# Kernel tuning notes

Hardware: AMD Instinct MI355X
Metric: run time of the kernel (lower is better)

The kernel has to match this reference:

```python
import jax, jax.numpy as jnp
import numpy as np
from jax import lax

WIN = 9
EPS = 1e-05


def _box_sum(v, win):
    # v: [B, 1, D, H, W]
    pad = win // 2
    dn = lax.conv_dimension_numbers(v.shape, (1, 1, win, win, win), ('NCDHW', 'OIDHW', 'NCDHW'))
    k = jnp.ones((win,), v.dtype)
    # apply 1D sum along D, H, W in turn
    v = lax.conv_general_dilated(v, k.reshape(1, 1, win, 1, 1), (1, 1, 1), [(pad, pad), (0, 0), (0, 0)], dimension_numbers=dn)
    v = lax.conv_general_dilated(v, k.reshape(1, 1, 1, win, 1), (1, 1, 1), [(0, 0), (pad, pad), (0, 0)], dimension_numbers=dn)
    v = lax.conv_general_dilated(v, k.reshape(1, 1, 1, 1, win), (1, 1, 1), [(0, 0), (0, 0), (pad, pad)], dimension_numbers=dn)
    return v


def setup_inputs() -> dict:
    key = jax.random.key(0)
    k1, k2 = jax.random.split(key)
    shape = (2, 1, 160, 192, 160)
    x = jax.random.uniform(k1, shape, dtype=jnp.float32)
    y = jax.random.uniform(k2, shape, dtype=jnp.float32)
    return {"x": x, "y": y}


def reference(x, y):
    win = WIN
    win_size = float(win ** 3)
    x_sum = _box_sum(x, win)
    y_sum = _box_sum(y, win)
    x2_sum = _box_sum(x * x, win)
    y2_sum = _box_sum(y * y, win)
    xy_sum = _box_sum(x * y, win)
    cross = xy_sum - x_sum * y_sum / win_size
    x_var = jnp.maximum(x2_sum - x_sum * x_sum / win_size, EPS)
    y_var = jnp.maximum(y2_sum - y_sum * y_sum / win_size, EPS)
    cc = cross * cross / (x_var * y_var)
    return -jnp.mean(cc)
```

## Files before the change

### kernel.cpp

```cpp
#include <hip/hip_runtime.h>

#define BB 2
#define DD 160
#define HH 192
#define WW 160
#define HW (HH * WW)
#define PAD 4
#define TH 16
#define TW 16
#define EXT 24
#define XSTR 28
#define PLANE 768
#define WCS 456
#define WJS 28
#define WPS (5 * WCS)
#define HWS 20
#define HCS2 324
#define CHUNK 55
#define NCH 3
#define NITER 63
#define WT (WW / TW)
#define HT (HH / TH)
#define NBLK (WT * HT * NCH * BB)
#define NTASK 288
#define EPS 1e-5f
#define INV_WS (1.0f / 729.0f)

__device__ __forceinline__ void bar_lgkm() {
  asm volatile("s_waitcnt lgkmcnt(0)" ::: "memory");
  __builtin_amdgcn_s_barrier();
  asm volatile("" ::: "memory");
}

__global__ void __launch_bounds__(256) k_lncc(
    const float* __restrict__ x, const float* __restrict__ y,
    float* __restrict__ partials)
{
  __shared__ __align__(16) float sbuf[2][PLANE];
  __shared__ __align__(16) float wsum[2 * WPS];
  __shared__ __align__(16) float hsum[5 * HCS2];
  __shared__ float red[4];

  const int t = threadIdx.x;
  const int w0 = blockIdx.x * TW;
  const int h0 = blockIdx.y * TH;
  const int bz = blockIdx.z;
  const int b = bz / NCH;
  const int chunk = bz - b * NCH;
  const int dc0 = chunk * CHUNK;
  const int g0 = dc0 - PAD;

  for (int i = t; i < 2 * PLANE; i += 256) (&sbuf[0][0])[i] = 0.f;

  int la0, la1; bool tk0, tk1;
  const float* gp0; const float* gp1;
  {
    const float* bx = x + (long)b * DD * HW;
    const float* by = y + (long)b * DD * HW;
#define MKTASK(TAU, LA, TK, GP)                                           \
    {                                                                     \
      int tau = (TAU);                                                    \
      int a = tau / 144;                                                  \
      int rem = tau - 144 * a;                                            \
      int r = rem / 6;                                                    \
      int q = rem - 6 * r;                                                \
      int aa = (a < 2) ? a : 0;                                           \
      int gh = h0 - PAD + r;                                              \
      int gw = w0 - PAD + 4 * q;                                          \
      bool ok = (tau < NTASK) && ((unsigned)gh < (unsigned)HH) &&         \
                ((unsigned)gw < (unsigned)WW);                            \
      LA = aa * PLANE + r * XSTR + 4 * q;                                 \
      TK = ok;                                                            \
      GP = (aa ? by : bx) + (ok ? (gh * WW + gw) : 0);                    \
    }
    MKTASK(t, la0, tk0, gp0)
    MKTASK(256 + t, la1, tk1, gp1)
#undef MKTASK
  }

  const int c2 = t / 24, r2 = t - c2 * 24;
  const int arrA = ((c2 == 1) || (c2 == 3)) ? 1 : 0;
  const bool needB = (c2 == 4);
  const bool sqA = (c2 == 2) || (c2 == 3);
  const int paOff = arrA * PLANE + r2 * XSTR;
  const int pbOff = PLANE + r2 * XSTR;
  const int wwOff = c2 * WCS + r2;

  const int tt = t - 128;
  const int c3 = (tt >= 0 ? tt : 0) / 16, w3 = (tt >= 0 ? tt : 0) & 15;
  const int wrOff = c3 * WCS + w3 * WJS;
  float* const hwr = &hsum[c3 * HCS2 + w3 * HWS];

  const int h4 = t >> 4, w4 = t & 15;
  const float* const hrd = &hsum[w4 * HWS + h4];

  float ring[9][5];
#pragma unroll
  for (int i = 0; i < 9; ++i)
#pragma unroll
    for (int c = 0; c < 5; ++c) ring[i][c] = 0.f;
  float run0 = 0.f, run1 = 0.f, run2 = 0.f, run3 = 0.f, run4 = 0.f, acc = 0.f;

  __syncthreads();

#define P2_BODY(PARBASE)                                                   \
  {                                                                        \
    const float* pa = &sbuf[0][0] + paOff;                                 \
    float4 A0 = *(const float4*)(pa);                                      \
    float4 A1 = *(const float4*)(pa + 4);                                  \
    float4 A2 = *(const float4*)(pa + 8);                                  \
    float4 A3 = *(const float4*)(pa + 12);                                 \
    float4 A4 = *(const float4*)(pa + 16);                                 \
    float4 A5 = *(const float4*)(pa + 20);                                 \
    float av[EXT];                                                         \
    av[0]=A0.x; av[1]=A0.y; av[2]=A0.z; av[3]=A0.w;                        \
    av[4]=A1.x; av[5]=A1.y; av[6]=A1.z; av[7]=A1.w;                        \
    av[8]=A2.x; av[9]=A2.y; av[10]=A2.z; av[11]=A2.w;                      \
    av[12]=A3.x; av[13]=A3.y; av[14]=A3.z; av[15]=A3.w;                    \
    av[16]=A4.x; av[17]=A4.y; av[18]=A4.z; av[19]=A4.w;                    \
    av[20]=A5.x; av[21]=A5.y; av[22]=A5.z; av[23]=A5.w;                    \
    float q[EXT];                                                          \
    if (needB) {                                                           \
      const float* pb = &sbuf[0][0] + pbOff;                               \
      float4 B0 = *(const float4*)(pb);                                    \
      float4 B1 = *(const float4*)(pb + 4);                                \
      float4 B2 = *(const float4*)(pb + 8);                                \
      float4 B3 = *(const float4*)(pb + 12);                               \
      float4 B4 = *(const float4*)(pb + 16);                               \
      float4 B5 = *(const float4*)(pb + 20);                               \
      q[0]=av[0]*B0.x; q[1]=av[1]*B0.y; q[2]=av[2]*B0.z; q[3]=av[3]*B0.w;  \
      q[4]=av[4]*B1.x; q[5]=av[5]*B1.y; q[6]=av[6]*B1.z; q[7]=av[7]*B1.w;  \
      q[8]=av[8]*B2.x; q[9]=av[9]*B2.y; q[10]=av[10]*B2.z;                 \
      q[11]=av[11]*B2.w;                                                   \
      q[12]=av[12]*B3.x; q[13]=av[13]*B3.y; q[14]=av[14]*B3.z;             \
      q[15]=av[15]*B3.w;                                                   \
      q[16]=av[16]*B4.x; q[17]=av[17]*B4.y; q[18]=av[18]*B4.z;             \
      q[19]=av[19]*B4.w;                                                   \
      q[20]=av[20]*B5.x; q[21]=av[21]*B5.y; q[22]=av[22]*B5.z;             \
      q[23]=av[23]*B5.w;                                                   \
    } else {                                                               \
      _Pragma("unroll")                                                    \
      for (int i = 0; i < EXT; ++i) q[i] = sqA ? av[i] * av[i] : av[i];    \
    }                                                                      \
    float s = ((q[0] + q[1]) + (q[2] + q[3])) +                            \
              ((q[4] + q[5]) + (q[6] + q[7])) + q[8];                      \
    float* wq = &wsum[(PARBASE) + wwOff];                                  \
    wq[0] = s;                                                             \
    _Pragma("unroll")                                                      \
    for (int j = 1; j < TW; ++j) {                                         \
      s += q[j + 8] - q[j - 1];                                            \
      wq[j * WJS] = s;                                                     \
    }                                                                      \
  }

  float4 st0 = make_float4(0, 0, 0, 0), st1 = st0;
  bool ps0 = false, ps1 = false;
  {
    if ((unsigned)g0 < (unsigned)DD) {
      const long so = (long)g0 * HW;
      if (tk0) *(float4*)&(&sbuf[0][0])[la0] = *(const float4*)(gp0 + so);
      if (tk1) *(float4*)&(&sbuf[0][0])[la1] = *(const float4*)(gp1 + so);
    }
    const int g1i = g0 + 1;
    const bool v1 = ((unsigned)g1i < (unsigned)DD);
    const long so1 = (long)g1i * HW;
    ps0 = tk0 && v1; if (ps0) st0 = *(const float4*)(gp0 + so1);
    ps1 = tk1 && v1; if (ps1) st1 = *(const float4*)(gp1 + so1);
  }
  __syncthreads();
  if (((unsigned)g0 < (unsigned)DD) && t < 120) P2_BODY(0)
  bar_lgkm();
  if (ps0) *(float4*)&(&sbuf[0][0])[la0] = st0;
  if (ps1) *(float4*)&(&sbuf[0][0])[la1] = st1;
  {
    const int gn = g0 + 2;
    const bool nv = (2 < NITER) && ((unsigned)gn < (unsigned)DD);
    const long so = (long)gn * HW;
    ps0 = tk0 && nv; if (ps0) st0 = *(const float4*)(gp0 + so);
    ps1 = tk1 && nv; if (ps1) st1 = *(const float4*)(gp1 + so);
  }
  bar_lgkm();

  for (int ko = 0; ko < 7; ++ko) {
#pragma unroll
    for (int jj = 0; jj < 9; ++jj) {
      const int m = ko * 9 + jj + 1;
      const int s = m - 1;

      if (t < 128) {
        if ((m < NITER) && ((unsigned)(g0 + m) < (unsigned)DD) && (t < 120))
          P2_BODY((m & 1) * WPS)
      } else {
        if (((unsigned)(g0 + s) < (unsigned)DD) && (tt < 80)) {
          const float* wrd = &wsum[(s & 1) * WPS + wrOff];
          float4 V0 = *(const float4*)(wrd);
          float4 V1 = *(const float4*)(wrd + 4);
          float4 V2 = *(const float4*)(wrd + 8);
          float4 V3 = *(const float4*)(wrd + 12);
          float4 V4 = *(const float4*)(wrd + 16);
          float4 V5 = *(const float4*)(wrd + 20);
          float v[EXT];
          v[0]=V0.x; v[1]=V0.y; v[2]=V0.z; v[3]=V0.w;
          v[4]=V1.x; v[5]=V1.y; v[6]=V1.z; v[7]=V1.w;
          v[8]=V2.x; v[9]=V2.y; v[10]=V2.z; v[11]=V2.w;
          v[12]=V3.x; v[13]=V3.y; v[14]=V3.z; v[15]=V3.w;
          v[16]=V4.x; v[17]=V4.y; v[18]=V4.z; v[19]=V4.w;
          v[20]=V5.x; v[21]=V5.y; v[22]=V5.z; v[23]=V5.w;
          float hv[TH];
          float sv = ((v[0] + v[1]) + (v[2] + v[3])) +
                     ((v[4] + v[5]) + (v[6] + v[7])) + v[8];
          hv[0] = sv;
#pragma unroll
          for (int h = 1; h < TH; ++h) {
            sv += v[h + 8] - v[h - 1];
            hv[h] = sv;
          }
          *(float4*)&hwr[0]  = make_float4(hv[0],  hv[1],  hv[2],  hv[3]);
          *(float4*)&hwr[4]  = make_float4(hv[4],  hv[5],  hv[6],  hv[7]);
          *(float4*)&hwr[8]  = make_float4(hv[8],  hv[9],  hv[10], hv[11]);
          *(float4*)&hwr[12] = make_float4(hv[12], hv[13], hv[14], hv[15]);
        }
      }

      bar_lgkm();

      float hv0 = 0.f, hv1 = 0.f, hv2 = 0.f, hv3 = 0.f, hv4 = 0.f;
      if ((unsigned)(g0 + s) < (unsigned)DD) {
        hv0 = hrd[0];
        hv1 = hrd[HCS2];
        hv2 = hrd[2 * HCS2];
        hv3 = hrd[3 * HCS2];
        hv4 = hrd[4 * HCS2];
      }
      if (ps0) *(float4*)&(&sbuf[0][0])[la0] = st0;
      if (ps1) *(float4*)&(&sbuf[0][0])[la1] = st1;
      {
        const int gn = g0 + m + 2;
        const bool nv = (m + 2 < NITER) && ((unsigned)gn < (unsigned)DD);
        const long so = (long)gn * HW;
        ps0 = tk0 && nv; if (ps0) st0 = *(const float4*)(gp0 + so);
        ps1 = tk1 && nv; if (ps1) st1 = *(const float4*)(gp1 + so);
      }

      run0 += hv0 - ring[jj][0]; ring[jj][0] = hv0;
      run1 += hv1 - ring[jj][1]; ring[jj][1] = hv1;
      run2 += hv2 - ring[jj][2]; ring[jj][2] = hv2;
      run3 += hv3 - ring[jj][3]; ring[jj][3] = hv3;
      run4 += hv4 - ring[jj][4]; ring[jj][4] = hv4;

      if (s >= 8) {
        const int d = dc0 + (s - 8);
        if (d < DD) {
          float cross = fmaf(-run0 * INV_WS, run1, run4);
          float xv = fmaxf(fmaf(-run0 * INV_WS, run0, run2), EPS);
          float yv = fmaxf(fmaf(-run1 * INV_WS, run1, run3), EPS);
          acc += (cross * cross) * __builtin_amdgcn_rcpf(xv * yv);
        }
      }

      bar_lgkm();
    }
  }

#pragma unroll
  for (int o = 32; o > 0; o >>= 1) acc += __shfl_down(acc, o);
  if ((t & 63) == 0) red[t >> 6] = acc;
  __syncthreads();
  if (t == 0) {
    int bid = (bz * HT + blockIdx.y) * WT + blockIdx.x;
    partials[bid] = (red[0] + red[1]) + (red[2] + red[3]);
  }
}

__global__ void __launch_bounds__(256) k_finalize(
    const float* __restrict__ partials, float* __restrict__ out)
{
  __shared__ double red[256];
  double s = 0.0;
  for (int i = threadIdx.x; i < NBLK; i += 256) s += (double)partials[i];
  red[threadIdx.x] = s;
  __syncthreads();
  for (int o = 128; o > 0; o >>= 1) {
    if (threadIdx.x < o) red[threadIdx.x] += red[threadIdx.x + o];
    __syncthreads();
  }
  if (threadIdx.x == 0) {
    const double Nvox = (double)BB * DD * HH * WW;
    out[0] = (float)(-red[0] / Nvox);
  }
}

extern "C" void kernel_launch(void* const* d_in, const int* in_sizes, int n_in,
                              void* d_out, int out_size, void* d_ws, size_t ws_size,
                              hipStream_t stream) {
  (void)in_sizes; (void)n_in; (void)out_size; (void)ws_size;
  const float* x = (const float*)d_in[0];
  const float* y = (const float*)d_in[1];
  float* out = (float*)d_out;
  float* partials = (float*)d_ws;

  dim3 grid(WT, HT, BB * NCH);
  k_lncc<<<grid, 256, 0, stream>>>(x, y, partials);
  k_finalize<<<1, 256, 0, stream>>>(partials, out);
}
```

Baseline: 69.59 us.

## Double-buffer staging and H-sum buffers to run a three-stage pipeline with one barrier

```diff
diff --git a/kernel.cpp b/kernel.cpp
--- a/kernel.cpp
+++ b/kernel.cpp
@@ -11,11 +11,13 @@
 #define EXT 24
 #define XSTR 28
 #define PLANE 768
+#define SB_PAR (2 * PLANE)
 #define WCS 456
 #define WJS 28
 #define WPS (5 * WCS)
 #define HWS 20
 #define HCS2 324
+#define HPS2 (5 * HCS2)
 #define CHUNK 55
 #define NCH 3
 #define NITER 63
@@ -36,9 +38,9 @@
     const float* __restrict__ x, const float* __restrict__ y,
     float* __restrict__ partials)
 {
-  __shared__ __align__(16) float sbuf[2][PLANE];
+  __shared__ __align__(16) float sbuf[2 * SB_PAR];
   __shared__ __align__(16) float wsum[2 * WPS];
-  __shared__ __align__(16) float hsum[5 * HCS2];
+  __shared__ __align__(16) float hsum[2 * HPS2];
   __shared__ float red[4];
 
   const int t = threadIdx.x;
@@ -50,7 +52,7 @@
   const int dc0 = chunk * CHUNK;
   const int g0 = dc0 - PAD;
 
-  for (int i = t; i < 2 * PLANE; i += 256) (&sbuf[0][0])[i] = 0.f;
+  for (int i = t; i < 2 * SB_PAR; i += 256) sbuf[i] = 0.f;
 
   int la0, la1; bool tk0, tk1;
   const float* gp0; const float* gp1;
@@ -89,10 +91,10 @@
   const int tt = t - 128;
   const int c3 = (tt >= 0 ? tt : 0) / 16, w3 = (tt >= 0 ? tt : 0) & 15;
   const int wrOff = c3 * WCS + w3 * WJS;
-  float* const hwr = &hsum[c3 * HCS2 + w3 * HWS];
+  const int hwOff = c3 * HCS2 + w3 * HWS;
 
   const int h4 = t >> 4, w4 = t & 15;
-  const float* const hrd = &hsum[w4 * HWS + h4];
+  const int hrOff = w4 * HWS + h4;
 
   float ring[9][5];
 #pragma unroll
@@ -103,9 +105,9 @@
 
   __syncthreads();
 
-#define P2_BODY(PARBASE)                                                   \
+#define P2_BODY(SBASE, WBASE)                                              \
   {                                                                        \
-    const float* pa = &sbuf[0][0] + paOff;                                 \
+    const float* pa = &sbuf[(SBASE) + paOff];                              \
     float4 A0 = *(const float4*)(pa);                                      \
     float4 A1 = *(const float4*)(pa + 4);                                  \
     float4 A2 = *(const float4*)(pa + 8);                                  \
@@ -121,7 +123,7 @@
     av[20]=A5.x; av[21]=A5.y; av[22]=A5.z; av[23]=A5.w;                    \
     float q[EXT];                                                          \
     if (needB) {                                                           \
-      const float* pb = &sbuf[0][0] + pbOff;                               \
+      const float* pb = &sbuf[(SBASE) + pbOff];                            \
       float4 B0 = *(const float4*)(pb);                                    \
       float4 B1 = *(const float4*)(pb + 4);                                \
       float4 B2 = *(const float4*)(pb + 8);                                \
@@ -144,7 +146,7 @@
     }                                                                      \
     float s = ((q[0] + q[1]) + (q[2] + q[3])) +                            \
               ((q[4] + q[5]) + (q[6] + q[7])) + q[8];                      \
-    float* wq = &wsum[(PARBASE) + wwOff];                                  \
+    float* wq = &wsum[(WBASE) + wwOff];                                    \
     wq[0] = s;                                                             \
     _Pragma("unroll")                                                      \
     for (int j = 1; j < TW; ++j) {                                         \
@@ -158,8 +160,8 @@
   {
     if ((unsigned)g0 < (unsigned)DD) {
       const long so = (long)g0 * HW;
-      if (tk0) *(float4*)&(&sbuf[0][0])[la0] = *(const float4*)(gp0 + so);
-      if (tk1) *(float4*)&(&sbuf[0][0])[la1] = *(const float4*)(gp1 + so);
+      if (tk0) *(float4*)&sbuf[la0] = *(const float4*)(gp0 + so);
+      if (tk1) *(float4*)&sbuf[la1] = *(const float4*)(gp1 + so);
     }
     const int g1i = g0 + 1;
     const bool v1 = ((unsigned)g1i < (unsigned)DD);
@@ -168,31 +170,35 @@
     ps1 = tk1 && v1; if (ps1) st1 = *(const float4*)(gp1 + so1);
   }
   __syncthreads();
-  if (((unsigned)g0 < (unsigned)DD) && t < 120) P2_BODY(0)
-  bar_lgkm();
-  if (ps0) *(float4*)&(&sbuf[0][0])[la0] = st0;
-  if (ps1) *(float4*)&(&sbuf[0][0])[la1] = st1;
-  {
-    const int gn = g0 + 2;
-    const bool nv = (2 < NITER) && ((unsigned)gn < (unsigned)DD);
-    const long so = (long)gn * HW;
-    ps0 = tk0 && nv; if (ps0) st0 = *(const float4*)(gp0 + so);
-    ps1 = tk1 && nv; if (ps1) st1 = *(const float4*)(gp1 + so);
-  }
-  bar_lgkm();
-
-  for (int ko = 0; ko < 7; ++ko) {
+
+  for (int ko = 0; ko < 8; ++ko) {
 #pragma unroll
     for (int jj = 0; jj < 9; ++jj) {
-      const int m = ko * 9 + jj + 1;
-      const int s = m - 1;
+      const int m = ko * 9 + jj;
+      const int parm = m & 1;
+
+      {
+        float* sb1 = &sbuf[(parm ^ 1) * SB_PAR];
+        if (ps0) *(float4*)&sb1[la0] = st0;
+        if (ps1) *(float4*)&sb1[la1] = st1;
+      }
+      {
+        const int gn = g0 + m + 2;
+        const bool nv = (m + 2 < NITER) && ((unsigned)gn < (unsigned)DD);
+        const long so = (long)gn * HW;
+        ps0 = tk0 && nv; if (ps0) st0 = *(const float4*)(gp0 + so);
+        ps1 = tk1 && nv; if (ps1) st1 = *(const float4*)(gp1 + so);
+      }
 
       if (t < 128) {
         if ((m < NITER) && ((unsigned)(g0 + m) < (unsigned)DD) && (t < 120))
-          P2_BODY((m & 1) * WPS)
+          P2_BODY(parm * SB_PAR, parm * WPS)
       } else {
-        if (((unsigned)(g0 + s) < (unsigned)DD) && (tt < 80)) {
-          const float* wrd = &wsum[(s & 1) * WPS + wrOff];
+        const int s3 = m - 1;
+        if ((m >= 1) && (s3 < NITER) &&
+            ((unsigned)(g0 + s3) < (unsigned)DD) && (tt < 80)) {
+          const int p3 = s3 & 1;
+          const float* wrd = &wsum[p3 * WPS + wrOff];
           float4 V0 = *(const float4*)(wrd);
           float4 V1 = *(const float4*)(wrd + 4);
           float4 V2 = *(const float4*)(wrd + 8);
@@ -215,41 +221,34 @@
             sv += v[h + 8] - v[h - 1];
             hv[h] = sv;
           }
-          *(float4*)&hwr[0]  = make_float4(hv[0],  hv[1],  hv[2],  hv[3]);
-          *(float4*)&hwr[4]  = make_float4(hv[4],  hv[5],  hv[6],  hv[7]);
-          *(float4*)&hwr[8]  = make_float4(hv[8],  hv[9],  hv[10], hv[11]);
-          *(float4*)&hwr[12] = make_float4(hv[12], hv[13], hv[14], hv[15]);
+          float* hq = &hsum[p3 * HPS2 + hwOff];
+          *(float4*)&hq[0]  = make_float4(hv[0],  hv[1],  hv[2],  hv[3]);
+          *(float4*)&hq[4]  = make_float4(hv[4],  hv[5],  hv[6],  hv[7]);
+          *(float4*)&hq[8]  = make_float4(hv[8],  hv[9],  hv[10], hv[11]);
+          *(float4*)&hq[12] = make_float4(hv[12], hv[13], hv[14], hv[15]);
         }
       }
 
-      bar_lgkm();
-
+      const int s4 = m - 2;
       float hv0 = 0.f, hv1 = 0.f, hv2 = 0.f, hv3 = 0.f, hv4 = 0.f;
-      if ((unsigned)(g0 + s) < (unsigned)DD) {
-        hv0 = hrd[0];
-        hv1 = hrd[HCS2];
-        hv2 = hrd[2 * HCS2];
-        hv3 = hrd[3 * HCS2];
-        hv4 = hrd[4 * HCS2];
-      }
-      if (ps0) *(float4*)&(&sbuf[0][0])[la0] = st0;
-      if (ps1) *(float4*)&(&sbuf[0][0])[la1] = st1;
+      if ((m >= 2) && (s4 < NITER) && ((unsigned)(g0 + s4) < (unsigned)DD)) {
+        const float* hb = &hsum[(s4 & 1) * HPS2 + hrOff];
+        hv0 = hb[0];
+        hv1 = hb[HCS2];
+        hv2 = hb[2 * HCS2];
+        hv3 = hb[3 * HCS2];
+        hv4 = hb[4 * HCS2];
+      }
       {
-        const int gn = g0 + m + 2;
-        const bool nv = (m + 2 < NITER) && ((unsigned)gn < (unsigned)DD);
-        const long so = (long)gn * HW;
-        ps0 = tk0 && nv; if (ps0) st0 = *(const float4*)(gp0 + so);
-        ps1 = tk1 && nv; if (ps1) st1 = *(const float4*)(gp1 + so);
-      }
-
-      run0 += hv0 - ring[jj][0]; ring[jj][0] = hv0;
-      run1 += hv1 - ring[jj][1]; ring[jj][1] = hv1;
-      run2 += hv2 - ring[jj][2]; ring[jj][2] = hv2;
-      run3 += hv3 - ring[jj][3]; ring[jj][3] = hv3;
-      run4 += hv4 - ring[jj][4]; ring[jj][4] = hv4;
-
-      if (s >= 8) {
-        const int d = dc0 + (s - 8);
+        const int rr = (jj + 7) % 9;
+        run0 += hv0 - ring[rr][0]; ring[rr][0] = hv0;
+        run1 += hv1 - ring[rr][1]; ring[rr][1] = hv1;
+        run2 += hv2 - ring[rr][2]; ring[rr][2] = hv2;
+        run3 += hv3 - ring[rr][3]; ring[rr][3] = hv3;
+        run4 += hv4 - ring[rr][4]; ring[rr][4] = hv4;
+      }
+      if ((s4 >= 8) && (s4 < NITER)) {
+        const int d = dc0 + (s4 - 8);
         if (d < DD) {
           float cross = fmaf(-run0 * INV_WS, run1, run4);
           float xv = fmaxf(fmaf(-run0 * INV_WS, run0, run2), EPS);
```

After: 69.52 us (median of 2 runs). About the same (-0.1%).
